# Optimization experiments

Measured on AMD Instinct MI355X. Metric: run time of the kernel, lower is better.

Reference implementation:

```python
import jax, jax.numpy as jnp
import numpy as np

L = 7
LVL = 3
B = 8
R = 16
N = 4 ** L  # 16384
P = N // 4  # number of local blocks
T = 4 * R   # ConvLocal output features


def build_permutation_indices(L, l):
    delta = 4 ** (L - l - 1)
    tmp = np.tile(np.arange(4) * delta, delta)
    tmp += np.repeat(np.arange(delta), 4)
    tmp = np.tile(tmp, 4 ** l)
    tmp += np.repeat(np.arange(4 ** l) * 4 ** (L - l), 4 ** (L - l))
    return jnp.asarray(tmp, dtype=jnp.int32)


def setup_inputs() -> dict:
    key = jax.random.key(0)
    kx, k1, k2, k3, k4 = jax.random.split(key, 5)
    scale = 1.0 / np.sqrt(T)
    x = jax.random.normal(kx, (B, 2, N, R), dtype=jnp.float32)
    # flax ConvLocal kernels: (out_spatial, kernel_size*in_features, features)
    W_rr = jax.random.normal(k1, (P, 4 * R, T), dtype=jnp.float32) * scale
    W_ri = jax.random.normal(k2, (P, 4 * R, T), dtype=jnp.float32) * scale
    W_ir = jax.random.normal(k3, (P, 4 * R, T), dtype=jnp.float32) * scale
    W_ii = jax.random.normal(k4, (P, 4 * R, T), dtype=jnp.float32) * scale
    perm_idx = build_permutation_indices(L, LVL)
    return {"x": x, "W_rr": W_rr, "W_ri": W_ri, "W_ir": W_ir,
            "W_ii": W_ii, "perm_idx": perm_idx}


def reference(x, W_rr, W_ri, W_ir, W_ii, perm_idx):
    b, _, n, r = x.shape
    p = n // 4
    # butterfly permutation gather along the spatial axis
    xp = jnp.take(x, perm_idx, axis=2)            # [B, 2, n, r]
    # group into length-4 windows; flax ConvLocal flattens (kernel, in_feat)
    xr = xp[:, 0].reshape(b, p, 4 * r)            # [B, p, 4r]
    xi = xp[:, 1].reshape(b, p, 4 * r)
    # block-diagonal (locally connected) matmuls, complex-style combine
    y_re = jnp.einsum('bpi,pio->bpo', xr, W_rr) + jnp.einsum('bpi,pio->bpo', xi, W_ri)
    y_im = jnp.einsum('bpi,pio->bpo', xr, W_ir) + jnp.einsum('bpi,pio->bpo', xi, W_ii)
    y = jnp.stack([y_re, y_im], axis=1)           # [B, 2, p, 4r]
    return y.reshape(b, 2, n, r)
```

## Files before the change

### kernel.cpp

```cpp
#include <hip/hip_runtime.h>
#include <stdint.h>

#define C_N 16384
#define C_R 16
#define C_P 4096
#define C_B 8

__global__ __launch_bounds__(128)
void butterfly_local_conv(const float* __restrict__ x,
                          const float* __restrict__ Wrr,
                          const float* __restrict__ Wri,
                          const float* __restrict__ Wir,
                          const float* __restrict__ Wii,
                          const int*   __restrict__ perm,
                          float* __restrict__ out)
{
    __shared__ float xs[2][C_B][64];

    const int t    = threadIdx.x;
    const int lane = t & 63;
    const int half = t >> 6;
    const int p    = blockIdx.x;

    #pragma unroll
    for (int j = 0; j < 2; ++j) {
        const int idx = t * 2 + j;
        const int c = idx >> 7;
        const int b = (idx >> 4) & 7;
        const int s = (idx >> 2) & 3;
        const int q = idx & 3;
        const int n = perm[4 * p + s];
        const float4 v =
            ((const float4*)(x + (((size_t)(b * 2 + c)) * C_N + n) * C_R))[q];
        *(float4*)&xs[c][b][s * 16 + q * 4] = v;
    }
    __syncthreads();

    const float* __restrict__ WA = (half ? Wir : Wrr) + (size_t)p * 4096 + lane;
    const float* __restrict__ WB = (half ? Wii : Wri) + (size_t)p * 4096 + lane;

    float acc[C_B] = {0.f, 0.f, 0.f, 0.f, 0.f, 0.f, 0.f, 0.f};

#define LOADC(A, Bv, cc)                                     \
    _Pragma("unroll")                                        \
    for (int k = 0; k < 4; ++k) {                            \
        A[k]  = WA[((cc) * 4 + k) * 64];                     \
        Bv[k] = WB[((cc) * 4 + k) * 64];                     \
    }

#define COMPC(A, Bv, cc)                                     \
    _Pragma("unroll")                                        \
    for (int b = 0; b < C_B; ++b) {                          \
        const float4 xr = *(const float4*)&xs[0][b][(cc)*4]; \
        const float4 xi = *(const float4*)&xs[1][b][(cc)*4]; \
        acc[b] = fmaf(xr.x, A[0],  acc[b]);                  \
        acc[b] = fmaf(xi.x, Bv[0], acc[b]);                  \
        acc[b] = fmaf(xr.y, A[1],  acc[b]);                  \
        acc[b] = fmaf(xi.y, Bv[1], acc[b]);                  \
        acc[b] = fmaf(xr.z, A[2],  acc[b]);                  \
        acc[b] = fmaf(xi.z, Bv[2], acc[b]);                  \
        acc[b] = fmaf(xr.w, A[3],  acc[b]);                  \
        acc[b] = fmaf(xi.w, Bv[3], acc[b]);                  \
    }

    float wa0[4], wb0[4], wa1[4], wb1[4];
    LOADC(wa0, wb0, 0);
    #pragma unroll
    for (int c = 0; c < 16; c += 2) {
        LOADC(wa1, wb1, c + 1);
        COMPC(wa0, wb0, c);
        if (c + 2 < 16) { LOADC(wa0, wb0, c + 2); }
        COMPC(wa1, wb1, c + 1);
    }
#undef LOADC
#undef COMPC

    const size_t obase = (size_t)p * 64 + lane;
    #pragma unroll
    for (int b = 0; b < C_B; ++b) {
        out[((size_t)(b * 2 + half)) * (C_N * C_R) + obase] = acc[b];
    }
}

extern "C" void kernel_launch(void* const* d_in, const int* in_sizes, int n_in,
                              void* d_out, int out_size, void* d_ws, size_t ws_size,
                              hipStream_t stream) {
    const float* x    = (const float*)d_in[0];
    const float* Wrr  = (const float*)d_in[1];
    const float* Wri  = (const float*)d_in[2];
    const float* Wir  = (const float*)d_in[3];
    const float* Wii  = (const float*)d_in[4];
    const int*   perm = (const int*)d_in[5];
    float* out = (float*)d_out;

    butterfly_local_conv<<<dim3(C_P), dim3(128), 0, stream>>>(
        x, Wrr, Wri, Wir, Wii, perm, out);
}
```

Before: 263.6 us.

## Vectorize weight loads as float4 with split-K across lane groups and shuffle reduce

Each lane now loads four consecutive weight columns as float4, and the 64 input rows are split across four lane groups that are reduced with cross-lane shuffles. Half of the weight loads are issued before the shared-memory barrier so they overlap the x gather. Outputs are written as float4, and the permutation is read with a single int4 load. This targets the weight-streaming bandwidth, which dominates, at the cost of more registers and shuffle reduction work.

```diff
diff --git a/kernel.cpp b/kernel.cpp
--- a/kernel.cpp
+++ b/kernel.cpp
@@ -21,7 +21,13 @@
     const int lane = t & 63;
     const int half = t >> 6;
     const int p    = blockIdx.x;
+    const int g    = lane >> 4;
+    const int m    = lane & 15;
 
+    const int4 pv = *(const int4*)(perm + 4 * p);
+
+    float4 xv[2];
+    int    lidx[2];
     #pragma unroll
     for (int j = 0; j < 2; ++j) {
         const int idx = t * 2 + j;
@@ -29,57 +35,69 @@
         const int b = (idx >> 4) & 7;
         const int s = (idx >> 2) & 3;
         const int q = idx & 3;
-        const int n = perm[4 * p + s];
-        const float4 v =
-            ((const float4*)(x + (((size_t)(b * 2 + c)) * C_N + n) * C_R))[q];
-        *(float4*)&xs[c][b][s * 16 + q * 4] = v;
+        const int n = (s & 2) ? ((s & 1) ? pv.w : pv.z)
+                              : ((s & 1) ? pv.y : pv.x);
+        xv[j] = ((const float4*)(x + (((size_t)(b * 2 + c)) * C_N + n) * C_R))[q];
+        lidx[j] = c * 512 + b * 64 + s * 16 + q * 4;
     }
+
+    const float* __restrict__ WAp = (half ? Wir : Wrr) + (size_t)p * 4096 + 4 * lane;
+    const float* __restrict__ WBp = (half ? Wii : Wri) + (size_t)p * 4096 + 4 * lane;
+
+    float4 A[8], B[8];
+    #pragma unroll
+    for (int j = 0; j < 8; ++j) {
+        A[j] = *(const float4*)(WAp + 256 * j);
+        B[j] = *(const float4*)(WBp + 256 * j);
+    }
+
+    *(float4*)((float*)xs + lidx[0]) = xv[0];
+    *(float4*)((float*)xs + lidx[1]) = xv[1];
     __syncthreads();
 
-    const float* __restrict__ WA = (half ? Wir : Wrr) + (size_t)p * 4096 + lane;
-    const float* __restrict__ WB = (half ? Wii : Wri) + (size_t)p * 4096 + lane;
+    float4 acc[C_B];
+    #pragma unroll
+    for (int b = 0; b < C_B; ++b) acc[b] = make_float4(0.f, 0.f, 0.f, 0.f);
 
-    float acc[C_B] = {0.f, 0.f, 0.f, 0.f, 0.f, 0.f, 0.f, 0.f};
+    const float* xsg = &xs[0][0][0] + g;
 
-#define LOADC(A, Bv, cc)                                     \
-    _Pragma("unroll")                                        \
-    for (int k = 0; k < 4; ++k) {                            \
-        A[k]  = WA[((cc) * 4 + k) * 64];                     \
-        Bv[k] = WB[((cc) * 4 + k) * 64];                     \
+    #pragma unroll
+    for (int j = 0; j < 16; ++j) {
+        const float4 a = A[j & 7];
+        const float4 w = B[j & 7];
+        #pragma unroll
+        for (int b = 0; b < C_B; ++b) {
+            const float xr = xsg[b * 64 + 4 * j];
+            const float xi = xsg[512 + b * 64 + 4 * j];
+            acc[b].x = fmaf(xr, a.x, acc[b].x);
+            acc[b].y = fmaf(xr, a.y, acc[b].y);
+            acc[b].z = fmaf(xr, a.z, acc[b].z);
+            acc[b].w = fmaf(xr, a.w, acc[b].w);
+            acc[b].x = fmaf(xi, w.x, acc[b].x);
+            acc[b].y = fmaf(xi, w.y, acc[b].y);
+            acc[b].z = fmaf(xi, w.z, acc[b].z);
+            acc[b].w = fmaf(xi, w.w, acc[b].w);
+        }
+        if (j + 8 < 16) {
+            A[j & 7] = *(const float4*)(WAp + 256 * (j + 8));
+            B[j & 7] = *(const float4*)(WBp + 256 * (j + 8));
+        }
     }
 
-#define COMPC(A, Bv, cc)                                     \
-    _Pragma("unroll")                                        \
-    for (int b = 0; b < C_B; ++b) {                          \
-        const float4 xr = *(const float4*)&xs[0][b][(cc)*4]; \
-        const float4 xi = *(const float4*)&xs[1][b][(cc)*4]; \
-        acc[b] = fmaf(xr.x, A[0],  acc[b]);                  \
-        acc[b] = fmaf(xi.x, Bv[0], acc[b]);                  \
-        acc[b] = fmaf(xr.y, A[1],  acc[b]);                  \
-        acc[b] = fmaf(xi.y, Bv[1], acc[b]);                  \
-        acc[b] = fmaf(xr.z, A[2],  acc[b]);                  \
-        acc[b] = fmaf(xi.z, Bv[2], acc[b]);                  \
-        acc[b] = fmaf(xr.w, A[3],  acc[b]);                  \
-        acc[b] = fmaf(xi.w, Bv[3], acc[b]);                  \
+    #pragma unroll
+    for (int b = 0; b < C_B; ++b) {
+        acc[b].x += __shfl_xor(acc[b].x, 16); acc[b].x += __shfl_xor(acc[b].x, 32);
+        acc[b].y += __shfl_xor(acc[b].y, 16); acc[b].y += __shfl_xor(acc[b].y, 32);
+        acc[b].z += __shfl_xor(acc[b].z, 16); acc[b].z += __shfl_xor(acc[b].z, 32);
+        acc[b].w += __shfl_xor(acc[b].w, 16); acc[b].w += __shfl_xor(acc[b].w, 32);
     }
 
-    float wa0[4], wb0[4], wa1[4], wb1[4];
-    LOADC(wa0, wb0, 0);
-    #pragma unroll
-    for (int c = 0; c < 16; c += 2) {
-        LOADC(wa1, wb1, c + 1);
-        COMPC(wa0, wb0, c);
-        if (c + 2 < 16) { LOADC(wa0, wb0, c + 2); }
-        COMPC(wa1, wb1, c + 1);
-    }
-#undef LOADC
-#undef COMPC
-
-    const size_t obase = (size_t)p * 64 + lane;
-    #pragma unroll
-    for (int b = 0; b < C_B; ++b) {
-        out[((size_t)(b * 2 + half)) * (C_N * C_R) + obase] = acc[b];
-    }
+    const float4 s0 = (g == 0) ? acc[0] : (g == 1) ? acc[2] : (g == 2) ? acc[4] : acc[6];
+    const float4 s1 = (g == 0) ? acc[1] : (g == 1) ? acc[3] : (g == 2) ? acc[5] : acc[7];
+    const size_t obase = (size_t)p * 64 + 4 * m;
+    const int b0 = g * 2;
+    *(float4*)(out + ((size_t)(b0 * 2 + half)) * (C_N * C_R) + obase) = s0;
+    *(float4*)(out + ((size_t)((b0 + 1) * 2 + half)) * (C_N * C_R) + obase) = s1;
 }
 
 extern "C" void kernel_launch(void* const* d_in, const int* in_sizes, int n_in,
```

After: 420.8 us. +59.7%, slower.
